# Performance work log

Measured on AMD Instinct MI355X. Metric: run time of the kernel, lower is better.

The kernel has to match this reference:

```python
import jax, jax.numpy as jnp
import numpy as np


def setup_inputs() -> dict:
    key = jax.random.key(0)
    ks = jax.random.split(key, 4)
    B, C, H, W = 4, 256, 64, 64
    Cq = C // 8
    s_in = 1.0 / np.sqrt(C)
    return {
        "x": jax.random.normal(ks[0], (B, C, H, W), dtype=jnp.float32),
        "Wq": jax.random.normal(ks[1], (Cq, C), dtype=jnp.float32) * s_in,
        "bq": jnp.zeros((Cq,), dtype=jnp.float32),
        "Wk": jax.random.normal(ks[2], (Cq, C), dtype=jnp.float32) * s_in,
        "bk": jnp.zeros((Cq,), dtype=jnp.float32),
        "Wv": jax.random.normal(ks[3], (C, C), dtype=jnp.float32) * s_in,
        "bv": jnp.zeros((C,), dtype=jnp.float32),
    }


def reference(x, Wq, bq, Wk, bk, Wv, bv):
    B, C, H, W = x.shape
    N = H * W
    xf = x.reshape(B, C, N)  # [B, C, N] tokens
    # 1x1 convs == per-token linear projections
    Q = jnp.einsum('qc,bcn->bqn', Wq, xf) + bq[None, :, None]  # [B, C/8, N]
    K = jnp.einsum('qc,bcn->bqn', Wk, xf) + bk[None, :, None]  # [B, C/8, N]
    V = jnp.einsum('vc,bcn->bvn', Wv, xf) + bv[None, :, None]  # [B, C,   N]
    # full self-attention over spatial tokens (no scaling, per original)
    scores = jnp.einsum('bdi,bdj->bij', Q, K)      # [B, N, N]
    attn = jax.nn.softmax(scores, axis=-1)
    out = jnp.einsum('bcj,bij->bci', V, attn)       # [B, C, N]
    return out.reshape(B, C, H, W) + x
```

## Files before the change

kernel.cpp:

```cpp
#include <hip/hip_runtime.h>

typedef short short8 __attribute__((ext_vector_type(8)));
typedef float f32x4 __attribute__((ext_vector_type(4)));
typedef unsigned short u16;
typedef u16 u16x8 __attribute__((ext_vector_type(8)));
typedef unsigned int u32;
typedef u32 u32x2 __attribute__((ext_vector_type(2)));
typedef u32 u32x4 __attribute__((ext_vector_type(4)));

#define NTOK 4096
#define CDIM 256
#define TQ 64
#define TJ 64
#define NT (NTOK / TJ)
#define LOG2E 1.44269504088896f

__device__ __forceinline__ u16 f2bf(float f) {
    unsigned u = __float_as_uint(f);
    unsigned r = (u + 0x7fffu + ((u >> 16) & 1u)) >> 16;
    return (u16)r;
}
__device__ __forceinline__ float bf2f(u16 h) { return __uint_as_float(((unsigned)h) << 16); }
__device__ __forceinline__ u32 pk_bf16(float a, float b) {
    u32 w;
    asm("v_cvt_pk_bf16_f32 %0, %1, %2" : "=v"(w) : "v"(a), "v"(b));
    return w;
}

__global__ __launch_bounds__(256)
void wconv(const float* __restrict__ Wq, const float* __restrict__ Wk,
           const float* __restrict__ Wv, u16* __restrict__ whi, u16* __restrict__ wlo) {
    const int row = blockIdx.x;
    const int col = threadIdx.x;
    float v;
    if (row < 32)       v = Wq[row * 256 + col];
    else if (row < 64)  v = Wk[(row - 32) * 256 + col];
    else                v = Wv[(row - 64) * 256 + col];
    u16 h = f2bf(v);
    whi[row * 256 + col] = h;
    wlo[row * 256 + col] = f2bf(v - bf2f(h));
}

__global__ __launch_bounds__(256, 1)
void proj_fused(const float* __restrict__ x,
                const u16* __restrict__ whi, const u16* __restrict__ wlo,
                const float* __restrict__ bq, const float* __restrict__ bk,
                const float* __restrict__ bv,
                u16* __restrict__ qhi, u16* __restrict__ qlo,
                u16* __restrict__ khi, u16* __restrict__ klo,
                u16* __restrict__ vbf) {
    __shared__ __attribute__((aligned(16))) u16 lxh[64][260];
    __shared__ __attribute__((aligned(16))) u16 lxl[64][260];
    const int b  = blockIdx.y;
    const int n0 = blockIdx.x * 64;
    const int t  = threadIdx.x;
    const int w  = t >> 6;
    const int l  = t & 63;
    const int cl = l & 15;
    const int kg = l >> 4;

    const int sn = (t & 15) * 4;
    const int sc = t >> 4;
#pragma unroll
    for (int cc = 0; cc < 16; cc++) {
        const int c = sc + cc * 16;
        const f32x4 xv = *(const f32x4*)&x[((size_t)(b * CDIM + c)) * NTOK + n0 + sn];
#pragma unroll
        for (int i = 0; i < 4; i++) {
            u16 hh = f2bf(xv[i]);
            lxh[sn + i][c] = hh;
            lxl[sn + i][c] = f2bf(xv[i] - bf2f(hh));
        }
    }
    __syncthreads();

    f32x4 acc[5][4];
    const f32x4 fz = {0.f, 0.f, 0.f, 0.f};
#pragma unroll
    for (int i = 0; i < 5; i++)
#pragma unroll
        for (int nt = 0; nt < 4; nt++) acc[i][nt] = fz;

#pragma unroll 2
    for (int ks = 0; ks < 8; ks++) {
        const int k0 = ks * 32;
        short8 bh[4], bl[4];
#pragma unroll
        for (int nt = 0; nt < 4; nt++) {
            bh[nt] = *(const short8*)&lxh[nt * 16 + cl][k0 + kg * 8];
            bl[nt] = *(const short8*)&lxl[nt * 16 + cl][k0 + kg * 8];
        }
#pragma unroll
        for (int i = 0; i < 5; i++) {
            const int mt = w * 5 + i;
            const size_t wb = (size_t)(mt * 16 + cl) * 256 + k0 + kg * 8;
            const short8 ah = *(const short8*)&whi[wb];
            const short8 al = *(const short8*)&wlo[wb];
#pragma unroll
            for (int nt = 0; nt < 4; nt++) {
                acc[i][nt] = __builtin_amdgcn_mfma_f32_16x16x32_bf16(ah, bh[nt], acc[i][nt], 0, 0, 0);
                acc[i][nt] = __builtin_amdgcn_mfma_f32_16x16x32_bf16(ah, bl[nt], acc[i][nt], 0, 0, 0);
                acc[i][nt] = __builtin_amdgcn_mfma_f32_16x16x32_bf16(al, bh[nt], acc[i][nt], 0, 0, 0);
            }
        }
    }

#pragma unroll
    for (int i = 0; i < 5; i++) {
        const int mt = w * 5 + i;
#pragma unroll
        for (int nt = 0; nt < 4; nt++) {
            const int n = n0 + nt * 16 + cl;
#pragma unroll
            for (int r = 0; r < 4; r++) {
                const int m = kg * 4 + r;
                float v = acc[i][nt][r];
                if (mt < 2) {
                    const int ch = mt * 16 + m;
                    v += bq[ch];
                    u16 hh = f2bf(v);
                    qhi[((size_t)(b * NTOK + n)) * 32 + ch] = hh;
                    qlo[((size_t)(b * NTOK + n)) * 32 + ch] = f2bf(v - bf2f(hh));
                } else if (mt < 4) {
                    const int ch = (mt - 2) * 16 + m;
                    v += bk[ch];
                    u16 hh = f2bf(v);
                    khi[((size_t)(b * NTOK + n)) * 32 + ch] = hh;
                    klo[((size_t)(b * NTOK + n)) * 32 + ch] = f2bf(v - bf2f(hh));
                } else {
                    const int c2 = (mt - 4) * 16 + m;
                    vbf[((size_t)(b * CDIM + c2)) * NTOK + n] = f2bf(v + bv[c2]);
                }
            }
        }
    }
}

__global__ __launch_bounds__(256, 2)
void attn_mfma(const u16* __restrict__ qhi, const u16* __restrict__ qlo,
               const u16* __restrict__ khi, const u16* __restrict__ klo,
               const u16* __restrict__ vbf, const float* __restrict__ x,
               float* __restrict__ out) {
    __shared__ __attribute__((aligned(16))) u16 lkh[2][TJ][32];
    __shared__ __attribute__((aligned(16))) u16 lkl[2][TJ][32];
    __shared__ __attribute__((aligned(16))) u16 lv[2][128][72];
    __shared__ __attribute__((aligned(16))) u32 lp[4][16][20];
    __shared__ __attribute__((aligned(16))) float lt[4][16][20];

    const int lin = blockIdx.x;
    const int p  = lin & 7;
    const int b  = p >> 1;
    const int h  = p & 1;
    const int qb = lin >> 3;
    const int i0 = qb * TQ;
    const int t  = threadIdx.x;
    const int w  = t >> 6;
    const int l  = t & 63;
    const int cl = l & 15;
    const int kg = l >> 4;

    const int iq = i0 + w * 16 + cl;
    const short8 qh = *(const short8*)&qhi[((size_t)(b * NTOK + iq)) * 32 + kg * 8];
    const short8 ql = *(const short8*)&qlo[((size_t)(b * NTOK + iq)) * 32 + kg * 8];

    const int vc    = t & 127;
    const int vhalf = t >> 7;
    const u16* vsrc = &vbf[((size_t)(b * CDIM + h * 128 + vc)) * NTOK + vhalf * 32];
    const int kj   = (t & 127) >> 1;
    const int kch2 = (t & 1) * 2;
    const u16* ksrcbase = (t < 128) ? khi : klo;
    const u16* ksrc = &ksrcbase[((size_t)(b * NTOK + kj)) * 32 + kch2 * 8];

    u16x8 vreg[4];
    u16x8 kreg0, kreg1;

    auto stage_load = [&](int tt) {
        const size_t j0 = (size_t)tt * TJ;
#pragma unroll
        for (int ch = 0; ch < 4; ch++)
            vreg[ch] = *(const u16x8*)&vsrc[j0 + ch * 8];
        kreg0 = *(const u16x8*)&ksrc[j0 * 32];
        kreg1 = *(const u16x8*)&ksrc[j0 * 32 + 8];
    };
    auto stage_write = [&](int buf) {
#pragma unroll
        for (int ch = 0; ch < 4; ch++)
            *(u16x8*)&lv[buf][vc][vhalf * 32 + ch * 8] = vreg[ch];
        const int swk = (kj >> 2) & 3;
        u16* kbase = (t < 128) ? &lkh[buf][kj][0] : &lkl[buf][kj][0];
        *(u16x8*)&kbase[((kch2)     ^ swk) * 8] = kreg0;
        *(u16x8*)&kbase[((kch2 + 1) ^ swk) * 8] = kreg1;
    };

    f32x4 acc[8];
    const f32x4 fz = {0.f, 0.f, 0.f, 0.f};
#pragma unroll
    for (int ct = 0; ct < 8; ct++) acc[ct] = fz;

    float m_r = -1.0e30f, l_r = 0.f;

    auto qkt_half = [&](int cur, int jtBase, f32x4& ra, f32x4& rb) {
        {
            const int row = jtBase * 16 + cl;
            const int ph  = (kg ^ ((row >> 2) & 3)) * 8;
            short8 kh = *(const short8*)&lkh[cur][row][ph];
            short8 kl = *(const short8*)&lkl[cur][row][ph];
            f32x4 sv = fz;
            sv = __builtin_amdgcn_mfma_f32_16x16x32_bf16(kh, qh, sv, 0, 0, 0);
            sv = __builtin_amdgcn_mfma_f32_16x16x32_bf16(kl, qh, sv, 0, 0, 0);
            sv = __builtin_amdgcn_mfma_f32_16x16x32_bf16(kh, ql, sv, 0, 0, 0);
            ra = sv;
        }
        {
            const int row = (jtBase + 1) * 16 + cl;
            const int ph  = (kg ^ ((row >> 2) & 3)) * 8;
            short8 kh = *(const short8*)&lkh[cur][row][ph];
            short8 kl = *(const short8*)&lkl[cur][row][ph];
            f32x4 sv = fz;
            sv = __builtin_amdgcn_mfma_f32_16x16x32_bf16(kh, qh, sv, 0, 0, 0);
            sv = __builtin_amdgcn_mfma_f32_16x16x32_bf16(kl, qh, sv, 0, 0, 0);
            sv = __builtin_amdgcn_mfma_f32_16x16x32_bf16(kh, ql, sv, 0, 0, 0);
            rb = sv;
        }
    };
    auto pv_half = [&](int buf, int ksOff, short8 pf) {
#pragma unroll
        for (int ct = 0; ct < 8; ct++) {
            const int row = ct * 16 + cl;
            short8 vb = *(const short8*)&lv[buf][row][ksOff + kg * 8];
            acc[ct] = __builtin_amdgcn_mfma_f32_16x16x32_bf16(vb, pf, acc[ct], 0, 0, 0);
        }
    };
    auto sm_half = [&](f32x4 sa, f32x4 sb) -> short8 {
        float tmax = fmaxf(fmaxf(fmaxf(sa[0], sa[1]), fmaxf(sa[2], sa[3])),
                           fmaxf(fmaxf(sb[0], sb[1]), fmaxf(sb[2], sb[3])));
        tmax = fmaxf(tmax, __shfl_xor(tmax, 16));
        tmax = fmaxf(tmax, __shfl_xor(tmax, 32));
        if (__any(tmax > m_r + 8.f)) {
            float mn = fmaxf(m_r, tmax);
            float f  = exp2f((m_r - mn) * LOG2E);
            m_r = mn;
            l_r *= f;
#pragma unroll
            for (int ct = 0; ct < 8; ct++) acc[ct] *= f;
        }
        const float mmv = m_r * LOG2E;
        float p0 = exp2f(fmaf(sa[0], LOG2E, -mmv));
        float p1 = exp2f(fmaf(sa[1], LOG2E, -mmv));
        float p2 = exp2f(fmaf(sa[2], LOG2E, -mmv));
        float p3 = exp2f(fmaf(sa[3], LOG2E, -mmv));
        float p4 = exp2f(fmaf(sb[0], LOG2E, -mmv));
        float p5 = exp2f(fmaf(sb[1], LOG2E, -mmv));
        float p6 = exp2f(fmaf(sb[2], LOG2E, -mmv));
        float p7 = exp2f(fmaf(sb[3], LOG2E, -mmv));
        l_r += ((p0 + p1) + (p2 + p3)) + ((p4 + p5) + (p6 + p7));
        u32x2 wA, wB;
        wA[0] = pk_bf16(p0, p1); wA[1] = pk_bf16(p2, p3);
        wB[0] = pk_bf16(p4, p5); wB[1] = pk_bf16(p6, p7);
        *(u32x2*)&lp[w][cl][2 * kg]     = wA;
        *(u32x2*)&lp[w][cl][8 + 2 * kg] = wB;
        return __builtin_bit_cast(short8, *(const u32x4*)&lp[w][cl][4 * kg]);
    };

    short8 pA, pcarry;
    f32x4 sa, sb;

    stage_load(0);
    stage_write(0);
    __syncthreads();

    stage_load(1);
    qkt_half(0, 0, sa, sb);
    pA = sm_half(sa, sb);
    __syncthreads();
    stage_write(1);
    __builtin_amdgcn_s_setprio(1);
    qkt_half(0, 2, sa, sb);
    pv_half(0, 0, pA);
    __builtin_amdgcn_s_setprio(0);
    pcarry = sm_half(sa, sb);
    __syncthreads();

    for (int tt = 1; tt < NT - 1; ++tt) {
        const int cur = tt & 1;
        const int nxt = cur ^ 1;

        stage_load(tt + 1);
        __builtin_amdgcn_s_setprio(1);
        qkt_half(cur, 0, sa, sb);
        pv_half(nxt, 32, pcarry);
        __builtin_amdgcn_s_setprio(0);
        pA = sm_half(sa, sb);
        __syncthreads();

        stage_write(nxt);
        __builtin_amdgcn_s_setprio(1);
        qkt_half(cur, 2, sa, sb);
        pv_half(cur, 0, pA);
        __builtin_amdgcn_s_setprio(0);
        pcarry = sm_half(sa, sb);
        __syncthreads();
    }

    {
        qkt_half(1, 0, sa, sb);
        pv_half(0, 32, pcarry);
        pA = sm_half(sa, sb);
        __syncthreads();
        qkt_half(1, 2, sa, sb);
        pv_half(1, 0, pA);
        pcarry = sm_half(sa, sb);
    }
    pv_half(1, 32, pcarry);

    l_r += __shfl_xor(l_r, 16);
    l_r += __shfl_xor(l_r, 32);
    const float linv = 1.f / l_r;
    const int c_r = l >> 2;
    const int q0  = (l & 3) * 4;
#pragma unroll
    for (int ct = 0; ct < 8; ct++) {
#pragma unroll
        for (int r = 0; r < 4; r++)
            lt[w][kg * 4 + r][cl] = acc[ct][r] * linv;
        const f32x4 vv = *(const f32x4*)&lt[w][c_r][q0];
        const int c = h * 128 + ct * 16 + c_r;
        const size_t base = ((size_t)(b * CDIM + c)) * NTOK + i0 + w * 16 + q0;
        const f32x4 xv = *(const f32x4*)&x[base];
        f32x4 o;
#pragma unroll
        for (int ii = 0; ii < 4; ii++) o[ii] = vv[ii] + xv[ii];
        *(f32x4*)&out[base] = o;
    }
}

extern "C" void kernel_launch(void* const* d_in, const int* in_sizes, int n_in,
                              void* d_out, int out_size, void* d_ws, size_t ws_size,
                              hipStream_t stream) {
    const float* x  = (const float*)d_in[0];
    const float* Wq = (const float*)d_in[1];
    const float* bq = (const float*)d_in[2];
    const float* Wk = (const float*)d_in[3];
    const float* bk = (const float*)d_in[4];
    const float* Wv = (const float*)d_in[5];
    const float* bv = (const float*)d_in[6];
    float* out = (float*)d_out;

    u16* qhi = (u16*)d_ws;
    u16* qlo = qhi + (size_t)4 * NTOK * 32;
    u16* khi = qlo + (size_t)4 * NTOK * 32;
    u16* klo = khi + (size_t)4 * NTOK * 32;
    u16* vbf = klo + (size_t)4 * NTOK * 32;
    u16* whi = vbf + (size_t)4 * CDIM * NTOK;
    u16* wlo = whi + (size_t)320 * 256;

    wconv<<<dim3(320), 256, 0, stream>>>(Wq, Wk, Wv, whi, wlo);
    proj_fused<<<dim3(64, 4), 256, 0, stream>>>(x, whi, wlo, bq, bk, bv,
                                                qhi, qlo, khi, klo, vbf);
    attn_mfma<<<dim3(512), 256, 0, stream>>>(qhi, qlo, khi, klo, vbf, x, out);
}
```

Before: 156.2 us.

## Repartition PV work so each wave owns channel slice across all query tiles

The PV matmul is reorganized so each wave computes 32 channels for all 64 queries, instead of all 128 channels for its own 16 queries. Each V fragment read from LDS is now reused across four P fragments, cutting LDS traffic for V. P tiles and per-row rescale factors are exchanged through double-buffered shared memory, and the row sums are shared at the end. The cost is extra cross-wave LDS traffic for P and the rescale factors, plus an additional barrier.

```diff
diff --git a/kernel.cpp b/kernel.cpp
--- a/kernel.cpp
+++ b/kernel.cpp
@@ -144,8 +144,10 @@
     __shared__ __attribute__((aligned(16))) u16 lkh[2][TJ][32];
     __shared__ __attribute__((aligned(16))) u16 lkl[2][TJ][32];
     __shared__ __attribute__((aligned(16))) u16 lv[2][128][72];
-    __shared__ __attribute__((aligned(16))) u32 lp[4][16][20];
+    __shared__ __attribute__((aligned(16))) u32 lp[2][4][16][20];
     __shared__ __attribute__((aligned(16))) float lt[4][16][20];
+    __shared__ float lfx[2][4][16];
+    __shared__ float lsc[4][16];
 
     const int lin = blockIdx.x;
     const int p  = lin & 7;
@@ -192,12 +194,15 @@
         *(u16x8*)&kbase[((kch2 + 1) ^ swk) * 8] = kreg1;
     };
 
-    f32x4 acc[8];
+    f32x4 acc[2][4];
     const f32x4 fz = {0.f, 0.f, 0.f, 0.f};
 #pragma unroll
-    for (int ct = 0; ct < 8; ct++) acc[ct] = fz;
+    for (int ct = 0; ct < 2; ct++)
+#pragma unroll
+        for (int qt = 0; qt < 4; qt++) acc[ct][qt] = fz;
 
     float m_r = -1.0e30f, l_r = 0.f;
+    const int crow0 = w * 32 + cl;
 
     auto qkt_half = [&](int cur, int jtBase, f32x4& ra, f32x4& rb) {
         {
@@ -223,27 +228,45 @@
             rb = sv;
         }
     };
-    auto pv_half = [&](int buf, int ksOff, short8 pf) {
-#pragma unroll
-        for (int ct = 0; ct < 8; ct++) {
-            const int row = ct * 16 + cl;
+    auto pv_half = [&](int buf, int ksOff, int par) {
+        short8 pf[4];
+#pragma unroll
+        for (int qt = 0; qt < 4; qt++)
+            pf[qt] = __builtin_bit_cast(short8, *(const u32x4*)&lp[par][qt][cl][4 * kg]);
+#pragma unroll
+        for (int ct = 0; ct < 2; ct++) {
+            const int row = crow0 + ct * 16;
             short8 vb = *(const short8*)&lv[buf][row][ksOff + kg * 8];
-            acc[ct] = __builtin_amdgcn_mfma_f32_16x16x32_bf16(vb, pf, acc[ct], 0, 0, 0);
-        }
-    };
-    auto sm_half = [&](f32x4 sa, f32x4 sb) -> short8 {
+#pragma unroll
+            for (int qt = 0; qt < 4; qt++)
+                acc[ct][qt] = __builtin_amdgcn_mfma_f32_16x16x32_bf16(vb, pf[qt], acc[ct][qt], 0, 0, 0);
+        }
+    };
+    auto rescale_from = [&](int par) {
+        f32x4 fq;
+#pragma unroll
+        for (int qt = 0; qt < 4; qt++) fq[qt] = lfx[par][qt][cl];
+        int ok = (fq[0] == 1.f) & (fq[1] == 1.f) & (fq[2] == 1.f) & (fq[3] == 1.f);
+        if (!__all(ok)) {
+#pragma unroll
+            for (int ct = 0; ct < 2; ct++)
+#pragma unroll
+                for (int qt = 0; qt < 4; qt++) acc[ct][qt] *= fq[qt];
+        }
+    };
+    auto sm_half = [&](int par, f32x4 sa, f32x4 sb) {
         float tmax = fmaxf(fmaxf(fmaxf(sa[0], sa[1]), fmaxf(sa[2], sa[3])),
                            fmaxf(fmaxf(sb[0], sb[1]), fmaxf(sb[2], sb[3])));
         tmax = fmaxf(tmax, __shfl_xor(tmax, 16));
         tmax = fmaxf(tmax, __shfl_xor(tmax, 32));
+        float f_r = 1.f;
         if (__any(tmax > m_r + 8.f)) {
             float mn = fmaxf(m_r, tmax);
-            float f  = exp2f((m_r - mn) * LOG2E);
+            f_r = exp2f((m_r - mn) * LOG2E);
             m_r = mn;
-            l_r *= f;
-#pragma unroll
-            for (int ct = 0; ct < 8; ct++) acc[ct] *= f;
-        }
+            l_r *= f_r;
+        }
+        if (kg == 0) lfx[par][w][cl] = f_r;
         const float mmv = m_r * LOG2E;
         float p0 = exp2f(fmaf(sa[0], LOG2E, -mmv));
         float p1 = exp2f(fmaf(sa[1], LOG2E, -mmv));
@@ -257,12 +280,10 @@
         u32x2 wA, wB;
         wA[0] = pk_bf16(p0, p1); wA[1] = pk_bf16(p2, p3);
         wB[0] = pk_bf16(p4, p5); wB[1] = pk_bf16(p6, p7);
-        *(u32x2*)&lp[w][cl][2 * kg]     = wA;
-        *(u32x2*)&lp[w][cl][8 + 2 * kg] = wB;
-        return __builtin_bit_cast(short8, *(const u32x4*)&lp[w][cl][4 * kg]);
-    };
-
-    short8 pA, pcarry;
+        *(u32x2*)&lp[par][w][cl][2 * kg]     = wA;
+        *(u32x2*)&lp[par][w][cl][8 + 2 * kg] = wB;
+    };
+
     f32x4 sa, sb;
 
     stage_load(0);
@@ -271,16 +292,18 @@
 
     stage_load(1);
     qkt_half(0, 0, sa, sb);
-    pA = sm_half(sa, sb);
+    sm_half(0, sa, sb);
     __syncthreads();
     stage_write(1);
     __builtin_amdgcn_s_setprio(1);
     qkt_half(0, 2, sa, sb);
-    pv_half(0, 0, pA);
+    rescale_from(0);
+    pv_half(0, 0, 0);
     __builtin_amdgcn_s_setprio(0);
-    pcarry = sm_half(sa, sb);
-    __syncthreads();
-
+    sm_half(1, sa, sb);
+    __syncthreads();
+
+#pragma unroll 2
     for (int tt = 1; tt < NT - 1; ++tt) {
         const int cur = tt & 1;
         const int nxt = cur ^ 1;
@@ -288,49 +311,62 @@
         stage_load(tt + 1);
         __builtin_amdgcn_s_setprio(1);
         qkt_half(cur, 0, sa, sb);
-        pv_half(nxt, 32, pcarry);
+        rescale_from(1);
+        pv_half(nxt, 32, 1);
         __builtin_amdgcn_s_setprio(0);
-        pA = sm_half(sa, sb);
+        sm_half(0, sa, sb);
         __syncthreads();
 
         stage_write(nxt);
         __builtin_amdgcn_s_setprio(1);
         qkt_half(cur, 2, sa, sb);
-        pv_half(cur, 0, pA);
+        rescale_from(0);
+        pv_half(cur, 0, 0);
         __builtin_amdgcn_s_setprio(0);
-        pcarry = sm_half(sa, sb);
+        sm_half(1, sa, sb);
         __syncthreads();
     }
 
-    {
-        qkt_half(1, 0, sa, sb);
-        pv_half(0, 32, pcarry);
-        pA = sm_half(sa, sb);
-        __syncthreads();
-        qkt_half(1, 2, sa, sb);
-        pv_half(1, 0, pA);
-        pcarry = sm_half(sa, sb);
-    }
-    pv_half(1, 32, pcarry);
+    qkt_half(1, 0, sa, sb);
+    rescale_from(1);
+    pv_half(0, 32, 1);
+    sm_half(0, sa, sb);
+    __syncthreads();
+    qkt_half(1, 2, sa, sb);
+    rescale_from(0);
+    pv_half(1, 0, 0);
+    sm_half(1, sa, sb);
+    __syncthreads();
+    rescale_from(1);
+    pv_half(1, 32, 1);
 
     l_r += __shfl_xor(l_r, 16);
     l_r += __shfl_xor(l_r, 32);
-    const float linv = 1.f / l_r;
+    if (kg == 0) lsc[w][cl] = l_r;
+    __syncthreads();
+
+    f32x4 linv;
+#pragma unroll
+    for (int qt = 0; qt < 4; qt++) linv[qt] = 1.f / lsc[qt][cl];
+
     const int c_r = l >> 2;
     const int q0  = (l & 3) * 4;
 #pragma unroll
-    for (int ct = 0; ct < 8; ct++) {
-#pragma unroll
-        for (int r = 0; r < 4; r++)
-            lt[w][kg * 4 + r][cl] = acc[ct][r] * linv;
-        const f32x4 vv = *(const f32x4*)&lt[w][c_r][q0];
-        const int c = h * 128 + ct * 16 + c_r;
-        const size_t base = ((size_t)(b * CDIM + c)) * NTOK + i0 + w * 16 + q0;
-        const f32x4 xv = *(const f32x4*)&x[base];
-        f32x4 o;
-#pragma unroll
-        for (int ii = 0; ii < 4; ii++) o[ii] = vv[ii] + xv[ii];
-        *(f32x4*)&out[base] = o;
+    for (int ct = 0; ct < 2; ct++) {
+#pragma unroll
+        for (int qt = 0; qt < 4; qt++) {
+#pragma unroll
+            for (int r = 0; r < 4; r++)
+                lt[w][kg * 4 + r][cl] = acc[ct][qt][r] * linv[qt];
+            const f32x4 vv = *(const f32x4*)&lt[w][c_r][q0];
+            const int c = h * 128 + w * 32 + ct * 16 + c_r;
+            const size_t base = ((size_t)(b * CDIM + c)) * NTOK + i0 + qt * 16 + q0;
+            const f32x4 xv = *(const f32x4*)&x[base];
+            f32x4 o;
+#pragma unroll
+            for (int ii = 0; ii < 4; ii++) o[ii] = vv[ii] + xv[ii];
+            *(f32x4*)&out[base] = o;
+        }
     }
 }
 
```

Measured after the change: 167.6 us. 7.3% more time.
